# Performance work log

Hardware: AMD Instinct MI355X
Metric: run time of the kernel (lower is better)

## Reference

```python
import jax, jax.numpy as jnp
import numpy as np

HEADS = 16
DIM_HEAD = 64
SCALE = DIM_HEAD ** -0.5
QUERY_DIM = 1024
CONTEXT_DIM = 1024
INNER = HEADS * DIM_HEAD


def setup_inputs() -> dict:
    key = jax.random.key(0)
    ks = jax.random.split(key, 8)
    B, N, M = 2, 1024, 4096
    x = jax.random.normal(ks[0], (B, N, QUERY_DIM), dtype=jnp.float32)
    context = jax.random.normal(ks[1], (B, M, CONTEXT_DIM), dtype=jnp.float32)
    importance_map = jax.random.normal(ks[2], (B, 1, 64, 64), dtype=jnp.float32)
    Wq = jax.random.normal(ks[3], (QUERY_DIM, INNER), dtype=jnp.float32) * 0.02
    Wk = jax.random.normal(ks[4], (CONTEXT_DIM, INNER), dtype=jnp.float32) * 0.02
    Wv = jax.random.normal(ks[5], (CONTEXT_DIM, INNER), dtype=jnp.float32) * 0.02
    Wo = jax.random.normal(ks[6], (INNER, QUERY_DIM), dtype=jnp.float32) * 0.02
    bo = jnp.zeros((QUERY_DIM,), dtype=jnp.float32)
    return {"x": x, "context": context, "importance_map": importance_map,
            "Wq": Wq, "Wk": Wk, "Wv": Wv, "Wo": Wo, "bo": bo}


def reference(x, context, importance_map, Wq, Wk, Wv, Wo, bo):
    B, N, _ = x.shape
    M = context.shape[1]
    h, d = HEADS, DIM_HEAD
    # projections, split heads: [B, h, n, d]
    q = (x @ Wq).reshape(B, N, h, d).transpose(0, 2, 1, 3)
    k = (context @ Wk).reshape(B, M, h, d).transpose(0, 2, 1, 3)
    v = (context @ Wv).reshape(B, M, h, d).transpose(0, 2, 1, 3)
    # scaled QK^T + additive importance bias (broadcast over heads & queries)
    sim = jnp.einsum('bhid,bhjd->bhij', q, k) * SCALE
    bias = importance_map.reshape(B, 1, 1, -1)  # [B,1,1,M]
    attn = jax.nn.softmax(sim + bias, axis=-1)
    out = jnp.einsum('bhij,bhjd->bhid', attn, v)
    out = out.transpose(0, 2, 1, 3).reshape(B, N, h * d)
    return out @ Wo + bo
```

## Files before the change

kernel.cpp:

```cpp
#include <hip/hip_runtime.h>
#include <stdint.h>


typedef float f32x4 __attribute__((ext_vector_type(4)));
typedef __bf16 bf16x8 __attribute__((ext_vector_type(8)));

#define SCALE 0.125f
#define LOG2E 1.4426950408889634f
#define N_Q 1024
#define M_KV 4096
#define KDIM 1024

static __device__ __forceinline__ unsigned short f2bf(float f) {
  union { float f; unsigned int u; } v; v.f = f;
  unsigned int r = v.u + 0x7fffu + ((v.u >> 16) & 1u);
  return (unsigned short)(r >> 16);
}
static __device__ __forceinline__ unsigned int cvtpk(float lo, float hi) {
  unsigned int r;
  asm("v_cvt_pk_bf16_f32 %0, %1, %2" : "=v"(r) : "v"(lo), "v"(hi));
  return r;
}
static __device__ __forceinline__ float exp2a(float x) {
  float r;
  asm("v_exp_f32 %0, %1" : "=v"(r) : "v"(x));
  return r;
}
static __device__ __forceinline__ void gload16(const void* g, void* l) {
  __builtin_amdgcn_global_load_lds(
      (const __attribute__((address_space(1))) void*)g,
      (__attribute__((address_space(3))) void*)l, 16, 0, 0);
}
static __device__ __forceinline__ void gload4(const void* g, void* l) {
  __builtin_amdgcn_global_load_lds(
      (const __attribute__((address_space(1))) void*)g,
      (__attribute__((address_space(3))) void*)l, 4, 0, 0);
}
static __device__ __forceinline__ void tile_fence() {
  asm volatile("s_waitcnt vmcnt(0)" ::: "memory");
  __builtin_amdgcn_s_barrier();
  __builtin_amdgcn_sched_barrier(0);
}

__global__ __launch_bounds__(256) void prep(const float* __restrict__ x,
                                            const float* __restrict__ ctx,
                                            const float* __restrict__ imp,
                                            unsigned short* __restrict__ xb,
                                            unsigned short* __restrict__ cb,
                                            float* __restrict__ impL) {
  const int NX = (2048 * 1024) / 4;
  const int NC = (8192 * 1024) / 4;
  const int NI = 8192 / 4;
  int i = blockIdx.x * 256 + threadIdx.x;
  int stride = gridDim.x * 256;
  for (; i < NX + NC + NI; i += stride) {
    if (i < NX) {
      float4 v = reinterpret_cast<const float4*>(x)[i];
      ushort4 o; o.x = f2bf(v.x); o.y = f2bf(v.y); o.z = f2bf(v.z); o.w = f2bf(v.w);
      reinterpret_cast<ushort4*>(xb)[i] = o;
    } else if (i < NX + NC) {
      int j = i - NX;
      float4 v = reinterpret_cast<const float4*>(ctx)[j];
      ushort4 o; o.x = f2bf(v.x); o.y = f2bf(v.y); o.z = f2bf(v.z); o.w = f2bf(v.w);
      reinterpret_cast<ushort4*>(cb)[j] = o;
    } else {
      int j = i - NX - NC;
      float4 v = reinterpret_cast<const float4*>(imp)[j];
      float4 o; o.x = v.x * LOG2E; o.y = v.y * LOG2E; o.z = v.z * LOG2E; o.w = v.w * LOG2E;
      reinterpret_cast<float4*>(impL)[j] = o;
    }
  }
}

__global__ __launch_bounds__(256) void tcvt4(const float* __restrict__ w0,
                                             const float* __restrict__ w1,
                                             const float* __restrict__ w2,
                                             const float* __restrict__ w3,
                                             unsigned short* __restrict__ o0,
                                             unsigned short* __restrict__ o1,
                                             unsigned short* __restrict__ o2,
                                             unsigned short* __restrict__ o3) {
  const int R = 1024, C = 1024;
  __shared__ float tile[32][33];
  const float* in; unsigned short* out;
  switch (blockIdx.z) {
    case 0: in = w0; out = o0; break;
    case 1: in = w1; out = o1; break;
    case 2: in = w2; out = o2; break;
    default: in = w3; out = o3; break;
  }
  int bx = blockIdx.x * 32, by = blockIdx.y * 32;
  int x = threadIdx.x & 31;
  int y0 = threadIdx.x >> 5;
  #pragma unroll
  for (int yy = y0; yy < 32; yy += 8)
    tile[yy][x] = in[(size_t)(by + yy) * C + bx + x];
  __syncthreads();
  #pragma unroll
  for (int yy = y0; yy < 32; yy += 8)
    out[(size_t)(bx + yy) * R + by + x] = f2bf(tile[x][yy]);
}

__global__ __launch_bounds__(256) void gemm_qkv(const unsigned short* __restrict__ xb,
                                                const unsigned short* __restrict__ cb,
                                                const unsigned short* __restrict__ Wqt,
                                                const unsigned short* __restrict__ Wkt,
                                                const unsigned short* __restrict__ Wvt,
                                                unsigned short* __restrict__ qa,
                                                unsigned short* __restrict__ ka,
                                                unsigned short* __restrict__ vtb) {
  const int LDT = 32;
  __shared__ __align__(16) unsigned short As[2][128 * LDT];
  __shared__ __align__(16) unsigned short Bs[2][128 * LDT];

  const int nwg = gridDim.x;
  const int lin = blockIdx.x;
  const int swz = (lin & 7) * (nwg >> 3) + (lin >> 3);

  int variant, m0, n0;
  if (swz < 128)      { variant = 0; m0 = (swz >> 3) * 128;        n0 = (swz & 7) * 128; }
  else if (swz < 640) { int r = swz - 128; variant = 1; m0 = (r >> 3) * 128; n0 = (r & 7) * 128; }
  else                { int r = swz - 640; variant = 2; m0 = (r >> 6) * 128; n0 = (r & 63) * 128; }
  const unsigned short* A  = (variant == 0) ? xb  : (variant == 1) ? cb  : Wvt;
  const unsigned short* Bt = (variant == 0) ? Wqt : (variant == 1) ? Wkt : cb;

  const int t = threadIdx.x;
  const int wave = t >> 6, lane = t & 63;
  const int wr = wave >> 1, wc = wave & 1;
  const int lrow = lane & 15, g = lane >> 4;

  f32x4 acc[4][4] = {};

  const int r16 = lane >> 2;
  const int c8 = (lane & 3) * 8;
  const int rb = wave * 32;

  auto STAGE = [&](int bi, int k0) {
    gload16(&A[(size_t)(m0 + rb + r16) * KDIM + k0 + c8],       &As[bi][rb * LDT]);
    gload16(&A[(size_t)(m0 + rb + 16 + r16) * KDIM + k0 + c8],  &As[bi][(rb + 16) * LDT]);
    gload16(&Bt[(size_t)(n0 + rb + r16) * KDIM + k0 + c8],      &Bs[bi][rb * LDT]);
    gload16(&Bt[(size_t)(n0 + rb + 16 + r16) * KDIM + k0 + c8], &Bs[bi][(rb + 16) * LDT]);
  };

  STAGE(0, 0);
  tile_fence();

  for (int k0 = 0; k0 < KDIM; k0 += 32) {
    const int buf = (k0 >> 5) & 1;
    if (k0 + 32 < KDIM) STAGE(buf ^ 1, k0 + 32);

    bf16x8 af[4], bfr[4];
    #pragma unroll
    for (int mi = 0; mi < 4; mi++)
      af[mi] = *reinterpret_cast<const bf16x8*>(&As[buf][(wr * 64 + mi * 16 + lrow) * LDT + g * 8]);
    #pragma unroll
    for (int ni = 0; ni < 4; ni++)
      bfr[ni] = *reinterpret_cast<const bf16x8*>(&Bs[buf][(wc * 64 + ni * 16 + lrow) * LDT + g * 8]);
    #pragma unroll
    for (int mi = 0; mi < 4; mi++)
      #pragma unroll
      for (int ni = 0; ni < 4; ni++)
        acc[mi][ni] = __builtin_amdgcn_mfma_f32_16x16x32_bf16(af[mi], bfr[ni], acc[mi][ni], 0, 0, 0);

    tile_fence();
  }

  #pragma unroll
  for (int mi = 0; mi < 4; mi++) {
    #pragma unroll
    for (int ni = 0; ni < 4; ni++) {
      #pragma unroll
      for (int r = 0; r < 4; r++) {
        int R = m0 + wr * 64 + mi * 16 + g * 4 + r;
        int Cc = n0 + wc * 64 + ni * 16 + lrow;
        unsigned short bv = f2bf(acc[mi][ni][r]);
        if (variant == 0) {
          int h = Cc >> 6, d = Cc & 63;
          int b = R >> 10, n = R & 1023;
          qa[(((size_t)(b * 16 + h)) * 1024 + n) * 64 + d] = bv;
        } else if (variant == 1) {
          int h = Cc >> 6, d = Cc & 63;
          int b = R >> 12, m = R & 4095;
          ka[(((size_t)(b * 16 + h)) * 4096 + m) * 64 + d] = bv;
        } else {
          int h = R >> 6, d = R & 63;
          int b = Cc >> 12, m = Cc & 4095;
          vtb[(((size_t)(b * 16 + h)) * 64 + d) * 4096 + m] = bv;
        }
      }
    }
  }
}

__global__ __launch_bounds__(256) void gemm_o(const unsigned short* __restrict__ A,
                                              const unsigned short* __restrict__ Bt,
                                              float* __restrict__ outp,
                                              const float* __restrict__ bias) {
  const int LDT = 32;
  __shared__ __align__(16) unsigned short As[2][128 * LDT];
  __shared__ __align__(16) unsigned short Bs[2][128 * LDT];

  const int nwg = gridDim.x;
  const int lin = blockIdx.x;
  const int swz = (lin & 7) * (nwg >> 3) + (lin >> 3);
  const int m0 = (swz >> 3) * 128;
  const int n0 = (swz & 7) * 128;

  const int t = threadIdx.x;
  const int wave = t >> 6, lane = t & 63;
  const int wr = wave >> 1, wc = wave & 1;
  const int lrow = lane & 15, g = lane >> 4;

  f32x4 acc[4][4] = {};

  const int r16 = lane >> 2;
  const int c8 = (lane & 3) * 8;
  const int rb = wave * 32;

  auto STAGE = [&](int bi, int k0) {
    gload16(&A[(size_t)(m0 + rb + r16) * KDIM + k0 + c8],       &As[bi][rb * LDT]);
    gload16(&A[(size_t)(m0 + rb + 16 + r16) * KDIM + k0 + c8],  &As[bi][(rb + 16) * LDT]);
    gload16(&Bt[(size_t)(n0 + rb + r16) * KDIM + k0 + c8],      &Bs[bi][rb * LDT]);
    gload16(&Bt[(size_t)(n0 + rb + 16 + r16) * KDIM + k0 + c8], &Bs[bi][(rb + 16) * LDT]);
  };

  STAGE(0, 0);
  tile_fence();

  for (int k0 = 0; k0 < KDIM; k0 += 32) {
    const int buf = (k0 >> 5) & 1;
    if (k0 + 32 < KDIM) STAGE(buf ^ 1, k0 + 32);

    bf16x8 af[4], bfr[4];
    #pragma unroll
    for (int mi = 0; mi < 4; mi++)
      af[mi] = *reinterpret_cast<const bf16x8*>(&As[buf][(wr * 64 + mi * 16 + lrow) * LDT + g * 8]);
    #pragma unroll
    for (int ni = 0; ni < 4; ni++)
      bfr[ni] = *reinterpret_cast<const bf16x8*>(&Bs[buf][(wc * 64 + ni * 16 + lrow) * LDT + g * 8]);
    #pragma unroll
    for (int mi = 0; mi < 4; mi++)
      #pragma unroll
      for (int ni = 0; ni < 4; ni++)
        acc[mi][ni] = __builtin_amdgcn_mfma_f32_16x16x32_bf16(af[mi], bfr[ni], acc[mi][ni], 0, 0, 0);

    tile_fence();
  }

  #pragma unroll
  for (int mi = 0; mi < 4; mi++)
    #pragma unroll
    for (int ni = 0; ni < 4; ni++)
      #pragma unroll
      for (int r = 0; r < 4; r++) {
        int R = m0 + wr * 64 + mi * 16 + g * 4 + r;
        int Cc = n0 + wc * 64 + ni * 16 + lrow;
        outp[(size_t)R * 1024 + Cc] = acc[mi][ni][r] + bias[Cc];
      }
}

__global__ __launch_bounds__(256, 4) void attn_kernel(const unsigned short* __restrict__ q,
                                                      const unsigned short* __restrict__ k,
                                                      const unsigned short* __restrict__ vt,
                                                      const float* __restrict__ impL,
                                                      float* __restrict__ acc_ws,
                                                      float* __restrict__ l_ws,
                                                      int split, int lsplit) {
  __shared__ __align__(16) unsigned short Ks[2][64 * 64];
  __shared__ __align__(16) unsigned short Vs[2][64 * 64];
  __shared__ __align__(16) float Bls[2][64];

  const int nwg = gridDim.x;
  const int lin = blockIdx.x;
  const int swz = (lin & 7) * (nwg >> 3) + (lin >> 3);
  const int sp = swz & (split - 1);
  const int tmp = swz >> lsplit;
  const int qt8 = tmp & 7;
  const int bh = tmp >> 3;
  const int t = threadIdx.x;
  const int wave = t >> 6, lane = t & 63;
  const int lrow = lane & 15, g = lane >> 4;
  const int q0 = qt8 * 128 + wave * 32;

  const unsigned short* qbase = q + ((size_t)bh * N_Q + q0) * 64;
  const char* kbase = (const char*)(k + (size_t)bh * M_KV * 64);
  const char* vbase = (const char*)(vt + (size_t)bh * 64 * M_KV);
  const float* ibase = impL + (size_t)(bh >> 4) * M_KV;

  const int rj = lane >> 3;
  const int cb = (lane & 7) * 16;
  const int cbsV  = cb ^ (rj << 4);
  const int cbsK0 = cb ^ ((rj & 3) << 4);
  const int cbsK1 = cb ^ (((rj & 3) | 4) << 4);
  const int row0 = wave * 16 + rj;
  const int row1 = row0 + 8;

  const int g2 = lrow >> 2, r4 = lrow & 3;
  const int krA = g2 * 8 + r4;
  const int vk = r4 | ((g2 & 1) << 2);
  const int offK0 = (g * 16) ^ (vk << 4);
  const int offK1 = (g * 16 + 64) ^ (vk << 4);
  const int swrV = (lrow & 7) << 4;
  const int offV0 = (g * 16) ^ swrV;
  const int offV1 = (g * 16 + 64) ^ swrV;

  bf16x8 qf[2][2];
  #pragma unroll
  for (int s = 0; s < 2; s++)
    #pragma unroll
    for (int ks = 0; ks < 2; ks++)
      qf[s][ks] = *reinterpret_cast<const bf16x8*>(&qbase[(size_t)(s * 16 + lrow) * 64 + ks * 32 + g * 8]);

  f32x4 acc[2][4] = {};
  f32x4 accL[2] = {};

  union { unsigned int u[4]; bf16x8 v; } onesU;
  onesU.u[0] = 0x3F803F80u; onesU.u[1] = 0x3F803F80u;
  onesU.u[2] = 0x3F803F80u; onesU.u[3] = 0x3F803F80u;

  const float S2 = SCALE * LOG2E;
  const int mspan = M_KV >> lsplit;
  const int mlo = sp * mspan;
  const int nt = mspan >> 6;

  auto STAGE = [&](int bi, int m0) {
    gload16(kbase + (size_t)(m0 + row0) * 128 + cbsK0, &Ks[bi][(wave * 16) * 64]);
    gload16(kbase + (size_t)(m0 + row1) * 128 + cbsK1, &Ks[bi][(wave * 16 + 8) * 64]);
    gload16(vbase + (size_t)row0 * 8192 + (size_t)m0 * 2 + cbsV, &Vs[bi][(wave * 16) * 64]);
    gload16(vbase + (size_t)row1 * 8192 + (size_t)m0 * 2 + cbsV, &Vs[bi][(wave * 16 + 8) * 64]);
    gload4((const char*)(ibase + m0) + lane * 4, &Bls[bi][0]);
  };

  STAGE(0, mlo);
  tile_fence();

  for (int tt = 0; tt < nt; ++tt) {
    const int cur = tt & 1;
    if (tt + 1 < nt) STAGE(cur ^ 1, mlo + (tt + 1) * 64);

    const char* K_ = (const char*)&Ks[cur][0];
    const char* V_ = (const char*)&Vs[cur][0];
    const float* B_ = &Bls[cur][0];

    bf16x8 pfr[2][2];
    #pragma unroll
    for (int h = 0; h < 2; h++) {
      const char* kp = K_ + (size_t)(h * 32 + krA) * 128;
      bf16x8 kA0 = *reinterpret_cast<const bf16x8*>(kp + offK0);
      bf16x8 kA1 = *reinterpret_cast<const bf16x8*>(kp + offK1);
      bf16x8 kB0 = *reinterpret_cast<const bf16x8*>(kp + 512 + offK0);
      bf16x8 kB1 = *reinterpret_cast<const bf16x8*>(kp + 512 + offK1);
      f32x4 bA = *reinterpret_cast<const f32x4*>(&B_[h * 32 + g * 8]);
      f32x4 bB = *reinterpret_cast<const f32x4*>(&B_[h * 32 + g * 8 + 4]);
      #pragma unroll
      for (int s = 0; s < 2; s++) {
        f32x4 sA = {}, sB = {};
        sA = __builtin_amdgcn_mfma_f32_16x16x32_bf16(kA0, qf[s][0], sA, 0, 0, 0);
        sA = __builtin_amdgcn_mfma_f32_16x16x32_bf16(kA1, qf[s][1], sA, 0, 0, 0);
        sB = __builtin_amdgcn_mfma_f32_16x16x32_bf16(kB0, qf[s][0], sB, 0, 0, 0);
        sB = __builtin_amdgcn_mfma_f32_16x16x32_bf16(kB1, qf[s][1], sB, 0, 0, 0);
        float pA[4], pB[4];
        #pragma unroll
        for (int r = 0; r < 4; r++) {
          pA[r] = exp2a(sA[r] * S2 + bA[r]);
          pB[r] = exp2a(sB[r] * S2 + bB[r]);
        }
        union { unsigned int u[4]; bf16x8 v; } pf;
        pf.u[0] = cvtpk(pA[0], pA[1]);
        pf.u[1] = cvtpk(pA[2], pA[3]);
        pf.u[2] = cvtpk(pB[0], pB[1]);
        pf.u[3] = cvtpk(pB[2], pB[3]);
        pfr[s][h] = pf.v;
      }
    }

    #pragma unroll
    for (int db = 0; db < 4; db++) {
      const char* vp = V_ + (size_t)(db * 16 + lrow) * 128;
      bf16x8 vf0 = *reinterpret_cast<const bf16x8*>(vp + offV0);
      bf16x8 vf1 = *reinterpret_cast<const bf16x8*>(vp + offV1);
      acc[0][db] = __builtin_amdgcn_mfma_f32_16x16x32_bf16(pfr[0][0], vf0, acc[0][db], 0, 0, 0);
      acc[0][db] = __builtin_amdgcn_mfma_f32_16x16x32_bf16(pfr[0][1], vf1, acc[0][db], 0, 0, 0);
      acc[1][db] = __builtin_amdgcn_mfma_f32_16x16x32_bf16(pfr[1][0], vf0, acc[1][db], 0, 0, 0);
      acc[1][db] = __builtin_amdgcn_mfma_f32_16x16x32_bf16(pfr[1][1], vf1, acc[1][db], 0, 0, 0);
    }
    accL[0] = __builtin_amdgcn_mfma_f32_16x16x32_bf16(pfr[0][0], onesU.v, accL[0], 0, 0, 0);
    accL[0] = __builtin_amdgcn_mfma_f32_16x16x32_bf16(pfr[0][1], onesU.v, accL[0], 0, 0, 0);
    accL[1] = __builtin_amdgcn_mfma_f32_16x16x32_bf16(pfr[1][0], onesU.v, accL[1], 0, 0, 0);
    accL[1] = __builtin_amdgcn_mfma_f32_16x16x32_bf16(pfr[1][1], onesU.v, accL[1], 0, 0, 0);

    tile_fence();
  }

  #pragma unroll
  for (int s = 0; s < 2; s++) {
    #pragma unroll
    for (int db = 0; db < 4; db++)
      #pragma unroll
      for (int r = 0; r < 4; r++) {
        size_t qrow = (size_t)bh * 1024 + q0 + s * 16 + g * 4 + r;
        acc_ws[(qrow * split + sp) * 64 + db * 16 + lrow] = acc[s][db][r];
      }
    if (lrow == 0) {
      #pragma unroll
      for (int r = 0; r < 4; r++)
        l_ws[((size_t)bh * 1024 + q0 + s * 16 + g * 4 + r) * split + sp] = accL[s][r];
    }
  }
}

__global__ __launch_bounds__(256) void attn_combine(const float* __restrict__ acc_ws,
                                                    const float* __restrict__ l_ws,
                                                    unsigned short* __restrict__ ao,
                                                    int split) {
  int bid = blockIdx.x;
  int bh = bid >> 4, qt = bid & 15;
  int b = bh >> 4, h = bh & 15;
  int t = threadIdx.x;
  int c4 = t & 15;
  int rbase = (t >> 4) * 4;

  #pragma unroll
  for (int rr = 0; rr < 4; rr++) {
    int row = rbase + rr;
    int qx = qt * 64 + row;
    f32x4 s = {};
    float ls = 0.f;
    for (int sp = 0; sp < split; sp++) {
      size_t idx = ((size_t)bh * 1024 + qx) * split + sp;
      const f32x4 a = *reinterpret_cast<const f32x4*>(&acc_ws[idx * 64 + c4 * 4]);
      s += a;
      ls += l_ws[idx];
    }
    float inv = 1.0f / ls;
    ushort4 o;
    o.x = f2bf(s[0] * inv);
    o.y = f2bf(s[1] * inv);
    o.z = f2bf(s[2] * inv);
    o.w = f2bf(s[3] * inv);
    size_t orow = (size_t)b * N_Q + qx;
    *reinterpret_cast<ushort4*>(&ao[orow * 1024 + h * 64 + c4 * 4]) = o;
  }
}

extern "C" void kernel_launch(void* const* d_in, const int* in_sizes, int n_in,
                              void* d_out, int out_size, void* d_ws, size_t ws_size,
                              hipStream_t stream) {
  const float* x   = (const float*)d_in[0];
  const float* ctx = (const float*)d_in[1];
  const float* imp = (const float*)d_in[2];
  const float* Wq  = (const float*)d_in[3];
  const float* Wk  = (const float*)d_in[4];
  const float* Wv  = (const float*)d_in[5];
  const float* Wo  = (const float*)d_in[6];
  const float* bo  = (const float*)d_in[7];
  float* out = (float*)d_out;

  unsigned short* xb  = (unsigned short*)d_ws;
  unsigned short* cb  = xb  + (size_t)2048 * 1024;
  unsigned short* Wqt = cb  + (size_t)8192 * 1024;
  unsigned short* Wkt = Wqt + (size_t)1024 * 1024;
  unsigned short* Wvt = Wkt + (size_t)1024 * 1024;
  unsigned short* Wot = Wvt + (size_t)1024 * 1024;
  unsigned short* qa  = Wot + (size_t)1024 * 1024;
  unsigned short* ka  = qa  + (size_t)2048 * 1024;
  unsigned short* vtb = ka  + (size_t)8192 * 1024;
  unsigned short* ao  = vtb + (size_t)8192 * 1024;
  float* impL = (float*)(ao + (size_t)2048 * 1024);
  size_t base_bytes = (size_t)((char*)(impL + 8192) - (char*)d_ws);

  size_t per_split = (size_t)32 * 1024 * 64 * 4 + (size_t)32 * 1024 * 4;
  int split = 1, lsplit = 0;
  if (ws_size >= base_bytes + 4 * per_split) { split = 4; lsplit = 2; }
  else if (ws_size >= base_bytes + 2 * per_split) { split = 2; lsplit = 1; }
  float* acc_ws = (float*)((char*)d_ws + base_bytes);
  float* l_ws   = (float*)((char*)d_ws + base_bytes + (size_t)split * 32 * 1024 * 64 * 4);

  prep<<<2048, 256, 0, stream>>>(x, ctx, imp, xb, cb, impL);
  tcvt4<<<dim3(32, 32, 4), 256, 0, stream>>>(Wq, Wk, Wv, Wo, Wqt, Wkt, Wvt, Wot);

  gemm_qkv<<<1152, 256, 0, stream>>>(xb, cb, Wqt, Wkt, Wvt, qa, ka, vtb);

  attn_kernel<<<dim3(256 * split), 256, 0, stream>>>(qa, ka, vtb, impL, acc_ws, l_ws, split, lsplit);
  attn_combine<<<512, 256, 0, stream>>>(acc_ws, l_ws, ao, split);

  gemm_o<<<128, 256, 0, stream>>>(ao, Wot, out, bo);
}
```

Measured before the change: 164.1 us.

## Triple-buffer GEMM LDS staging with swizzled layout and reordered V-projection tiles

Both projection GEMMs move from double to triple buffering in LDS. Each iteration prefetches two tiles ahead and waits only on the older group (vmcnt(4)), so global loads overlap compute across more iterations. An XOR swizzle is applied to the 16-byte chunk placement to cut LDS bank conflicts on the MFMA fragment reads. The V-transpose tile order is changed so consecutive workgroups share context columns. LDS use grows by half, which may lower occupancy, and the vmcnt(4) wait relies on exactly four loads being outstanding per stage.

```diff
diff --git a/kernel.cpp b/kernel.cpp
--- a/kernel.cpp
+++ b/kernel.cpp
@@ -36,7 +36,12 @@
       (const __attribute__((address_space(1))) void*)g,
       (__attribute__((address_space(3))) void*)l, 4, 0, 0);
 }
-static __device__ __forceinline__ void tile_fence() {
+static __device__ __forceinline__ void fence4() {
+  asm volatile("s_waitcnt vmcnt(4)" ::: "memory");
+  __builtin_amdgcn_s_barrier();
+  __builtin_amdgcn_sched_barrier(0);
+}
+static __device__ __forceinline__ void fence0() {
   asm volatile("s_waitcnt vmcnt(0)" ::: "memory");
   __builtin_amdgcn_s_barrier();
   __builtin_amdgcn_sched_barrier(0);
@@ -110,8 +115,8 @@
                                                 unsigned short* __restrict__ ka,
                                                 unsigned short* __restrict__ vtb) {
   const int LDT = 32;
-  __shared__ __align__(16) unsigned short As[2][128 * LDT];
-  __shared__ __align__(16) unsigned short Bs[2][128 * LDT];
+  __shared__ __align__(16) unsigned short As[3][128 * LDT];
+  __shared__ __align__(16) unsigned short Bs[3][128 * LDT];
 
   const int nwg = gridDim.x;
   const int lin = blockIdx.x;
@@ -120,7 +125,7 @@
   int variant, m0, n0;
   if (swz < 128)      { variant = 0; m0 = (swz >> 3) * 128;        n0 = (swz & 7) * 128; }
   else if (swz < 640) { int r = swz - 128; variant = 1; m0 = (r >> 3) * 128; n0 = (r & 7) * 128; }
-  else                { int r = swz - 640; variant = 2; m0 = (r >> 6) * 128; n0 = (r & 63) * 128; }
+  else                { int r = swz - 640; variant = 2; m0 = (r & 7) * 128;  n0 = (r >> 3) * 128; }
   const unsigned short* A  = (variant == 0) ? xb  : (variant == 1) ? cb  : Wvt;
   const unsigned short* Bt = (variant == 0) ? Wqt : (variant == 1) ? Wkt : cb;
 
@@ -132,37 +137,46 @@
   f32x4 acc[4][4] = {};
 
   const int r16 = lane >> 2;
-  const int c8 = (lane & 3) * 8;
+  const int cs8 = (((lane & 3) ^ ((r16 >> 1) & 3)) * 8);
   const int rb = wave * 32;
+  const int gsw = (g ^ ((lrow >> 1) & 3)) * 8;
 
   auto STAGE = [&](int bi, int k0) {
-    gload16(&A[(size_t)(m0 + rb + r16) * KDIM + k0 + c8],       &As[bi][rb * LDT]);
-    gload16(&A[(size_t)(m0 + rb + 16 + r16) * KDIM + k0 + c8],  &As[bi][(rb + 16) * LDT]);
-    gload16(&Bt[(size_t)(n0 + rb + r16) * KDIM + k0 + c8],      &Bs[bi][rb * LDT]);
-    gload16(&Bt[(size_t)(n0 + rb + 16 + r16) * KDIM + k0 + c8], &Bs[bi][(rb + 16) * LDT]);
+    gload16(&A[(size_t)(m0 + rb + r16) * KDIM + k0 + cs8],       &As[bi][rb * LDT]);
+    gload16(&A[(size_t)(m0 + rb + 16 + r16) * KDIM + k0 + cs8],  &As[bi][(rb + 16) * LDT]);
+    gload16(&Bt[(size_t)(n0 + rb + r16) * KDIM + k0 + cs8],      &Bs[bi][rb * LDT]);
+    gload16(&Bt[(size_t)(n0 + rb + 16 + r16) * KDIM + k0 + cs8], &Bs[bi][(rb + 16) * LDT]);
   };
-
-  STAGE(0, 0);
-  tile_fence();
-
-  for (int k0 = 0; k0 < KDIM; k0 += 32) {
-    const int buf = (k0 >> 5) & 1;
-    if (k0 + 32 < KDIM) STAGE(buf ^ 1, k0 + 32);
-
+  auto COMPUTE = [&](int buf) {
     bf16x8 af[4], bfr[4];
     #pragma unroll
     for (int mi = 0; mi < 4; mi++)
-      af[mi] = *reinterpret_cast<const bf16x8*>(&As[buf][(wr * 64 + mi * 16 + lrow) * LDT + g * 8]);
+      af[mi] = *reinterpret_cast<const bf16x8*>(&As[buf][(wr * 64 + mi * 16 + lrow) * LDT + gsw]);
     #pragma unroll
     for (int ni = 0; ni < 4; ni++)
-      bfr[ni] = *reinterpret_cast<const bf16x8*>(&Bs[buf][(wc * 64 + ni * 16 + lrow) * LDT + g * 8]);
+      bfr[ni] = *reinterpret_cast<const bf16x8*>(&Bs[buf][(wc * 64 + ni * 16 + lrow) * LDT + gsw]);
     #pragma unroll
     for (int mi = 0; mi < 4; mi++)
       #pragma unroll
       for (int ni = 0; ni < 4; ni++)
         acc[mi][ni] = __builtin_amdgcn_mfma_f32_16x16x32_bf16(af[mi], bfr[ni], acc[mi][ni], 0, 0, 0);
-
-    tile_fence();
+  };
+
+  STAGE(0, 0);
+  STAGE(1, 32);
+  fence4();
+
+  int it = 0;
+  for (int k0 = 0; k0 < KDIM; k0 += 32, ++it) {
+    const int buf = it % 3;
+    if (k0 + 64 < KDIM) {
+      STAGE((it + 2) % 3, k0 + 64);
+      COMPUTE(buf);
+      fence4();
+    } else {
+      COMPUTE(buf);
+      fence0();
+    }
   }
 
   #pragma unroll
@@ -197,8 +211,8 @@
                                               float* __restrict__ outp,
                                               const float* __restrict__ bias) {
   const int LDT = 32;
-  __shared__ __align__(16) unsigned short As[2][128 * LDT];
-  __shared__ __align__(16) unsigned short Bs[2][128 * LDT];
+  __shared__ __align__(16) unsigned short As[3][128 * LDT];
+  __shared__ __align__(16) unsigned short Bs[3][128 * LDT];
 
   const int nwg = gridDim.x;
   const int lin = blockIdx.x;
@@ -214,37 +228,46 @@
   f32x4 acc[4][4] = {};
 
   const int r16 = lane >> 2;
-  const int c8 = (lane & 3) * 8;
+  const int cs8 = (((lane & 3) ^ ((r16 >> 1) & 3)) * 8);
   const int rb = wave * 32;
+  const int gsw = (g ^ ((lrow >> 1) & 3)) * 8;
 
   auto STAGE = [&](int bi, int k0) {
-    gload16(&A[(size_t)(m0 + rb + r16) * KDIM + k0 + c8],       &As[bi][rb * LDT]);
-    gload16(&A[(size_t)(m0 + rb + 16 + r16) * KDIM + k0 + c8],  &As[bi][(rb + 16) * LDT]);
-    gload16(&Bt[(size_t)(n0 + rb + r16) * KDIM + k0 + c8],      &Bs[bi][rb * LDT]);
-    gload16(&Bt[(size_t)(n0 + rb + 16 + r16) * KDIM + k0 + c8], &Bs[bi][(rb + 16) * LDT]);
+    gload16(&A[(size_t)(m0 + rb + r16) * KDIM + k0 + cs8],       &As[bi][rb * LDT]);
+    gload16(&A[(size_t)(m0 + rb + 16 + r16) * KDIM + k0 + cs8],  &As[bi][(rb + 16) * LDT]);
+    gload16(&Bt[(size_t)(n0 + rb + r16) * KDIM + k0 + cs8],      &Bs[bi][rb * LDT]);
+    gload16(&Bt[(size_t)(n0 + rb + 16 + r16) * KDIM + k0 + cs8], &Bs[bi][(rb + 16) * LDT]);
   };
-
-  STAGE(0, 0);
-  tile_fence();
-
-  for (int k0 = 0; k0 < KDIM; k0 += 32) {
-    const int buf = (k0 >> 5) & 1;
-    if (k0 + 32 < KDIM) STAGE(buf ^ 1, k0 + 32);
-
+  auto COMPUTE = [&](int buf) {
     bf16x8 af[4], bfr[4];
     #pragma unroll
     for (int mi = 0; mi < 4; mi++)
-      af[mi] = *reinterpret_cast<const bf16x8*>(&As[buf][(wr * 64 + mi * 16 + lrow) * LDT + g * 8]);
+      af[mi] = *reinterpret_cast<const bf16x8*>(&As[buf][(wr * 64 + mi * 16 + lrow) * LDT + gsw]);
     #pragma unroll
     for (int ni = 0; ni < 4; ni++)
-      bfr[ni] = *reinterpret_cast<const bf16x8*>(&Bs[buf][(wc * 64 + ni * 16 + lrow) * LDT + g * 8]);
+      bfr[ni] = *reinterpret_cast<const bf16x8*>(&Bs[buf][(wc * 64 + ni * 16 + lrow) * LDT + gsw]);
     #pragma unroll
     for (int mi = 0; mi < 4; mi++)
       #pragma unroll
       for (int ni = 0; ni < 4; ni++)
         acc[mi][ni] = __builtin_amdgcn_mfma_f32_16x16x32_bf16(af[mi], bfr[ni], acc[mi][ni], 0, 0, 0);
-
-    tile_fence();
+  };
+
+  STAGE(0, 0);
+  STAGE(1, 32);
+  fence4();
+
+  int it = 0;
+  for (int k0 = 0; k0 < KDIM; k0 += 32, ++it) {
+    const int buf = it % 3;
+    if (k0 + 64 < KDIM) {
+      STAGE((it + 2) % 3, k0 + 64);
+      COMPUTE(buf);
+      fence4();
+    } else {
+      COMPUTE(buf);
+      fence0();
+    }
   }
 
   #pragma unroll
@@ -332,7 +355,7 @@
   };
 
   STAGE(0, mlo);
-  tile_fence();
+  fence0();
 
   for (int tt = 0; tt < nt; ++tt) {
     const int cur = tt & 1;
@@ -389,7 +412,7 @@
     accL[1] = __builtin_amdgcn_mfma_f32_16x16x32_bf16(pfr[1][0], onesU.v, accL[1], 0, 0, 0);
     accL[1] = __builtin_amdgcn_mfma_f32_16x16x32_bf16(pfr[1][1], onesU.v, accL[1], 0, 0, 0);
 
-    tile_fence();
+    fence0();
   }
 
   #pragma unroll
```

Result: slower. 192.9 us (median of 4 runs) (+17.6%).
